# Optimization experiments

Measured on AMD Instinct MI355X. Metric: run time of the kernel, lower is better.

Reference implementation:

```python
import jax, jax.numpy as jnp
import numpy as np

N_ORDERS = 2
CHUNK = 64            # real tokens per chunk
LINEAR_ACTIVATION = False
STAB = 10000.0


def _ensure_stability(x):
    x = jnp.clip(x, -STAB, STAB)
    return jnp.nan_to_num(x, nan=0.0, posinf=STAB, neginf=-STAB)


def setup_inputs() -> dict:
    key = jax.random.key(0)
    k1, k2, k3, k4 = jax.random.split(key, 4)
    B, H, NC, D = 2, 16, 32, 128
    CT = CHUNK * N_ORDERS  # 128 virtual tokens per chunk
    s = 1.0 / np.sqrt(D)
    q_chunks = jax.random.normal(k1, (B, H, NC, CT, D), jnp.float32) * s
    W = jax.random.normal(k2, (B, H, NC, CT, D), jnp.float32) * s
    U = jax.random.normal(k3, (B, H, NC, CT, D), jnp.float32) * s
    h0 = jax.random.normal(k4, (B, H, D, D), jnp.float32) * s
    return {"q_chunks": q_chunks, "W": W, "U": U, "h0": h0}


def _gelu_norm(h):
    # h_norm/2 * gelu(2*h/h_norm, tanh) applied to chunk-boundary state
    n = jnp.linalg.norm(h, axis=-1, keepdims=True) + 1e-6
    return n / 2.0 * jax.nn.gelu(2.0 * h / n, approximate=True)


def _delta_product_scan(q_chunks, W, U, h0):
    B, H, NC, CT, D = q_chunks.shape
    C = CT // N_ORDERS

    def body(h, chunk):
        q_c, w_c, u_c = chunk  # each [B,H,CT,D]
        # virtual-token layout: token c, step s lives at index c*n_orders+s
        qs = q_c.reshape(B, H, C, N_ORDERS, D)
        ws = w_c.reshape(B, H, C, N_ORDERS, D)
        us = u_c.reshape(B, H, C, N_ORDERS, D)
        state = jnp.broadcast_to(h[:, :, None], (B, H, C, D, D))  # per-token state
        outs = []
        for step in range(N_ORDERS):
            q_s = qs[:, :, :, step]
            w_s = ws[:, :, :, step]
            u_s = us[:, :, :, step]
            k_trans_h = jnp.einsum('bhcd,bhcde->bhce', w_s, state)
            u_val = u_s - k_trans_h
            o_inter = jnp.einsum('bhcd,bhcde->bhce', q_s, state)
            o_intra = q_s * u_val  # elementwise, as in source
            outs.append(o_intra + o_inter)
            state = _ensure_stability(state + w_s[..., :, None] * u_val[..., None, :])
        out = jnp.stack(outs, axis=3).reshape(B, H, CT, D)
        h_new = state[:, :, -1]
        if not LINEAR_ACTIVATION:
            h_new = _gelu_norm(h_new)
        return h_new, out

    chunks = (jnp.moveaxis(q_chunks, 2, 0), jnp.moveaxis(W, 2, 0), jnp.moveaxis(U, 2, 0))
    h_final, ys = jax.lax.scan(body, h0, chunks)
    return jnp.moveaxis(ys, 0, 2), h_final  # [B,H,NC,CT,D], [B,H,D,D]


def reference(q_chunks, W, U, h0):
    return _delta_product_scan(q_chunks, W, U, h0)
```

## Files before the change

### kernel.cpp

```cpp
#include <hip/hip_runtime.h>


#define Dd 128
#define NCH 32
#define YS 16777216

typedef __attribute__((ext_vector_type(4))) float floatx4;
typedef __attribute__((ext_vector_type(8))) short short8;

__device__ __forceinline__ unsigned cvtpk(float lo, float hi) {
  unsigned r;
  asm("v_cvt_pk_bf16_f32 %0, %1, %2" : "=v"(r) : "v"(lo), "v"(hi));
  return r;
}

__global__ __launch_bounds__(512) void p1_scan(const float* __restrict__ W,
    const float* __restrict__ U, const float* __restrict__ h0,
    unsigned short* __restrict__ hws, float* __restrict__ out) {
  __shared__ float wpre[NCH * 320];
  __shared__ float upre[NCH * 2 * Dd];
  __shared__ float d10pre[NCH];
  __shared__ float sqb[Dd * 129];
  __shared__ float nrm2[4 * 40];

  const int bh = blockIdx.x;
  const int t = threadIdx.x;
  const int w = t >> 6, l = t & 63;
  const int c = (w << 4) | (l & 15);
  const int rg = l >> 4;

  {
    const float* Wg = W + (size_t)bh * NCH * 16384;
    const float* Ug = U + (size_t)bh * NCH * 16384;
#pragma unroll
    for (int k = 0; k < 4; k++) {
      int idx4 = k * 512 + t;
      int n = idx4 >> 6;
      int rem = idx4 & 63;
      int r = rem >> 5, e4 = (rem & 31) * 4;
      size_t g = (size_t)n * 16384 + (size_t)(126 + r) * Dd + e4;
      *(float4*)&upre[idx4 * 4] = *(const float4*)&Ug[g];
      *(float4*)&wpre[n * 320 + r * 160 + (e4 >> 5) * 40 + (e4 & 31)] =
          *(const float4*)&Wg[g];
    }
  }
  {
    const float4* hg = (const float4*)(h0 + (size_t)bh * 16384);
#pragma unroll
    for (int k = 0; k < 8; k++) {
      int idx4 = k * 512 + t;
      float4 v = hg[idx4];
      int d = idx4 >> 5, e4 = (idx4 & 31) * 4;
      sqb[d * 129 + e4 + 0] = v.x;
      sqb[d * 129 + e4 + 1] = v.y;
      sqb[d * 129 + e4 + 2] = v.z;
      sqb[d * 129 + e4 + 3] = v.w;
    }
  }
  __syncthreads();
  {
    int n = t >> 4, j = t & 15;
    const float* w0p = &wpre[n * 320 + (j >> 2) * 40 + (j & 3) * 8];
    const float* w1p = w0p + 160;
    float p = 0.f;
#pragma unroll
    for (int i = 0; i < 8; i++) p += w0p[i] * w1p[i];
    p += __shfl_xor(p, 1, 64);
    p += __shfl_xor(p, 2, 64);
    p += __shfl_xor(p, 4, 64);
    p += __shfl_xor(p, 8, 64);
    if (j == 0) d10pre[n] = p;
  }
  float hr[32];
#pragma unroll
  for (int i = 0; i < 32; i++) hr[i] = sqb[(rg * 32 + i) * 129 + c];
  __syncthreads();

  const int cpos = (c & 96) | ((c + 8 * rg) & 31);
  float* sqw = &sqb[rg * 32 * 129 + cpos];
  const int srow = t >> 2, sst = t & 3;
  const float* sqr = &sqb[srow * 129 + sst * 32];

  unsigned short* hwsb = hws + (size_t)bh * NCH * 16384;
  {
    unsigned pk[16];
#pragma unroll
    for (int i = 0; i < 16; i++) pk[i] = cvtpk(hr[2 * i], hr[2 * i + 1]);
    uint4* dst = (uint4*)(hwsb + (size_t)c * Dd + rg * 32);
    dst[0] = make_uint4(pk[0], pk[1], pk[2], pk[3]);
    dst[1] = make_uint4(pk[4], pk[5], pk[6], pk[7]);
    dst[2] = make_uint4(pk[8], pk[9], pk[10], pk[11]);
    dst[3] = make_uint4(pk[12], pk[13], pk[14], pk[15]);
  }

  for (int n = 0; n < NCH; n++) {
    floatx4 w0v[8], w1v[8];
    const float* wb = &wpre[n * 320 + rg * 40];
#pragma unroll
    for (int i = 0; i < 8; i++) {
      w0v[i] = *(const floatx4*)&wb[4 * i];
      w1v[i] = *(const floatx4*)&wb[160 + 4 * i];
    }
    float a0 = 0.f, a1 = 0.f, b0 = 0.f, b1 = 0.f;
#pragma unroll
    for (int i = 0; i < 8; i += 2) {
#pragma unroll
      for (int j = 0; j < 4; j++) {
        float h0v = hr[4 * i + j];
        float h1v = hr[4 * i + 4 + j];
        a0 = fmaf(w0v[i][j], h0v, a0);
        a1 = fmaf(w1v[i][j], h0v, a1);
        b0 = fmaf(w0v[i + 1][j], h1v, b0);
        b1 = fmaf(w1v[i + 1][j], h1v, b1);
      }
    }
    a0 += b0; a1 += b1;
    a0 += __shfl_xor(a0, 16, 64);
    a0 += __shfl_xor(a0, 32, 64);
    a1 += __shfl_xor(a1, 16, 64);
    a1 += __shfl_xor(a1, 32, 64);
    const float u0 = upre[n * 256 + c];
    const float u1 = upre[n * 256 + Dd + c];
    const float d10 = d10pre[n];
    const float uv0 = u0 - a0;
    const float uv1 = u1 - a1 - d10 * uv0;
#pragma unroll
    for (int i = 0; i < 8; i++)
#pragma unroll
      for (int j = 0; j < 4; j++) {
        int ii = 4 * i + j;
        float s = __builtin_amdgcn_fmed3f(fmaf(w0v[i][j], uv0, hr[ii]),
                                          -10000.0f, 10000.0f);
        s = __builtin_amdgcn_fmed3f(fmaf(w1v[i][j], uv1, s),
                                    -10000.0f, 10000.0f);
        hr[ii] = s;
        sqw[ii * 129] = s;
      }
    __syncthreads();
    {
      float acc = 0.f, acc2 = 0.f;
#pragma unroll
      for (int b = 0; b < 4; b++) {
        const float* p = sqr + 8 * ((b + sst) & 3);
#pragma unroll
        for (int i = 0; i < 8; i += 2) {
          float v = p[i], v2 = p[i + 1];
          acc = fmaf(v, v, acc);
          acc2 = fmaf(v2, v2, acc2);
        }
      }
      acc += acc2;
      acc += __shfl_xor(acc, 1, 64);
      acc += __shfl_xor(acc, 2, 64);
      if (sst == 0) {
        float nd = sqrtf(acc) + 1e-6f;
        nrm2[(srow >> 5) * 40 + (srow & 31)] = __fdividef(2.0f, nd);
      }
    }
    __syncthreads();
    floatx4 r2v[8];
    const float* nb = &nrm2[rg * 40];
#pragma unroll
    for (int i = 0; i < 8; i++) r2v[i] = *(const floatx4*)&nb[4 * i];
#pragma unroll
    for (int i = 0; i < 8; i++)
#pragma unroll
      for (int j = 0; j < 4; j++) {
        int ii = 4 * i + j;
        float h = hr[ii];
        float x = h * r2v[i][j];
        float x2 = x * x;
        float aa = x * fmaf(0.071354816f, x2, 1.59576912f);
        float ex = __expf(-aa);
        hr[ii] = __fdividef(h, 1.0f + ex);
      }
    if (n < NCH - 1) {
      unsigned pk[16];
#pragma unroll
      for (int i = 0; i < 16; i++) pk[i] = cvtpk(hr[2 * i], hr[2 * i + 1]);
      uint4* dst = (uint4*)(hwsb + (size_t)(n + 1) * 16384 + (size_t)c * Dd + rg * 32);
      dst[0] = make_uint4(pk[0], pk[1], pk[2], pk[3]);
      dst[1] = make_uint4(pk[4], pk[5], pk[6], pk[7]);
      dst[2] = make_uint4(pk[8], pk[9], pk[10], pk[11]);
      dst[3] = make_uint4(pk[12], pk[13], pk[14], pk[15]);
    } else {
      float* ob = out + YS + (size_t)bh * 16384;
#pragma unroll
      for (int i = 0; i < 32; i++) ob[(rg * 32 + i) * Dd + c] = hr[i];
    }
  }
}

__global__ __launch_bounds__(512) void p2_out(const float* __restrict__ Q,
    const float* __restrict__ W, const float* __restrict__ U,
    const unsigned short* __restrict__ hws, float* __restrict__ out) {
  __shared__ unsigned short hT[Dd * 136];
  __shared__ float d10s[64], dq1s[64];
  __shared__ float dps[512];

  const int bid = blockIdx.x;
  const int n = bid & 31, bh = bid >> 5;
  const size_t base = (size_t)(bh * NCH + n) * 16384;
  const float* Qb = Q + base;
  const float* Wb = W + base;
  const float* Ub = U + base;
  float* Ob = out + base;
  const int t = threadIdx.x;

  {
    const uint4* src = (const uint4*)(hws + base);
#pragma unroll
    for (int i = 0; i < 4; i++) {
      int idx = t + i * 512;
      uint4 v = src[idx];
      int e = idx >> 4, j = idx & 15;
      *(uint4*)&hT[e * 136 + j * 8] = v;
    }
  }
  {
    int which = t >> 8, tt = t & 255;
    int cc = tt >> 2, part = tt & 3;
    const float4* ar = (const float4*)((which ? Qb : Wb) + (2 * cc + 1) * Dd + part * 32);
    const float4* w0r = (const float4*)(Wb + (2 * cc) * Dd + part * 32);
    float s = 0.f;
#pragma unroll
    for (int i = 0; i < 8; i++) {
      float4 a = ar[i], b = w0r[i];
      s += a.x * b.x + a.y * b.y + a.z * b.z + a.w * b.w;
    }
    dps[which * 256 + tt] = s;
  }
  __syncthreads();
  if (t < 128) {
    int which = t >> 6, cc = t & 63;
    const float* p = dps + which * 256 + cc * 4;
    float s = p[0] + p[1] + p[2] + p[3];
    (which ? dq1s : d10s)[cc] = s;
  }

  const int wv = t >> 6, l = t & 63;
  const int pr = wv >> 2, eq = wv & 3;
  const int lm = l & 15, lq = l >> 4;

  floatx4 acc[2][4][2];
#pragma unroll
  for (int m = 0; m < 2; m++)
#pragma unroll
    for (int ci = 0; ci < 4; ci++)
#pragma unroll
      for (int j = 0; j < 2; j++) acc[m][ci][j] = (floatx4){0.f, 0.f, 0.f, 0.f};

  for (int kc = 0; kc < 4; kc++) {
    const int k0 = kc * 32;
    short8 bfr[2];
#pragma unroll
    for (int j = 0; j < 2; j++) {
      int ee = (2 * eq + j) * 16 + lm;
      bfr[j] = *(const short8*)&hT[ee * 136 + k0 + 8 * lq];
    }
#pragma unroll
    for (int m = 0; m < 2; m++) {
      const float* X = m ? Wb : Qb;
#pragma unroll
      for (int ci = 0; ci < 4; ci++) {
        int cc = ci * 16 + lm;
        const float* row = X + (size_t)(2 * cc + pr) * Dd + k0 + 8 * lq;
        float4 f0 = ((const float4*)row)[0];
        float4 f1 = ((const float4*)row)[1];
        union { short8 v; unsigned u[4]; } af;
        af.u[0] = cvtpk(f0.x, f0.y);
        af.u[1] = cvtpk(f0.z, f0.w);
        af.u[2] = cvtpk(f1.x, f1.y);
        af.u[3] = cvtpk(f1.z, f1.w);
        acc[m][ci][0] = __builtin_amdgcn_mfma_f32_16x16x32_bf16(af.v, bfr[0], acc[m][ci][0], 0, 0, 0);
        acc[m][ci][1] = __builtin_amdgcn_mfma_f32_16x16x32_bf16(af.v, bfr[1], acc[m][ci][1], 0, 0, 0);
      }
    }
  }
  __syncthreads();
  float* uv0s = (float*)hT;

  if (pr == 0) {
#pragma unroll
    for (int ci = 0; ci < 4; ci++)
#pragma unroll
      for (int j = 0; j < 2; j++) {
        int ee = (2 * eq + j) * 16 + lm;
#pragma unroll
        for (int r = 0; r < 4; r++) {
          int cc = ci * 16 + lq * 4 + r;
          float T0 = acc[1][ci][j][r];
          float Q0h = acc[0][ci][j][r];
          float u0 = Ub[(2 * cc) * Dd + ee];
          float q0 = Qb[(2 * cc) * Dd + ee];
          float uv0 = u0 - T0;
          uv0s[cc * Dd + ee] = uv0;
          Ob[(2 * cc) * Dd + ee] = q0 * uv0 + Q0h;
        }
      }
  }
  __syncthreads();
  if (pr == 1) {
#pragma unroll
    for (int ci = 0; ci < 4; ci++)
#pragma unroll
      for (int j = 0; j < 2; j++) {
        int ee = (2 * eq + j) * 16 + lm;
#pragma unroll
        for (int r = 0; r < 4; r++) {
          int cc = ci * 16 + lq * 4 + r;
          float T1 = acc[1][ci][j][r];
          float Q1h = acc[0][ci][j][r];
          float u1 = Ub[(2 * cc + 1) * Dd + ee];
          float q1 = Qb[(2 * cc + 1) * Dd + ee];
          float uv0 = uv0s[cc * Dd + ee];
          float uv1 = u1 - T1 - d10s[cc] * uv0;
          Ob[(2 * cc + 1) * Dd + ee] = q1 * uv1 + Q1h + dq1s[cc] * uv0;
        }
      }
  }
}

extern "C" void kernel_launch(void* const* d_in, const int* in_sizes, int n_in,
                              void* d_out, int out_size, void* d_ws, size_t ws_size,
                              hipStream_t stream) {
  const float* Q = (const float*)d_in[0];
  const float* W = (const float*)d_in[1];
  const float* U = (const float*)d_in[2];
  const float* h0 = (const float*)d_in[3];
  float* out = (float*)d_out;
  unsigned short* hws = (unsigned short*)d_ws;

  p1_scan<<<32, 512, 0, stream>>>(W, U, h0, hws, out);
  p2_out<<<1024, 512, 0, stream>>>(Q, W, U, hws, out);
}
```

Baseline: 425.7 us.

## Double-buffer Q/W slices into LDS via async global_load_lds in p2_out

The p2_out matmul loop now stages Q and W k-slices into swizzled LDS buffers with async global-to-LDS loads, double-buffered so the next slice loads while the current one feeds MFMA. The odd-row waves now recompute the even-row uv0 with an extra MFMA accumulator instead of exchanging it through shared memory, which removes a block barrier. The aim is to hide global load latency and cut the sync. In exchange it uses more LDS, forces one block per CU through launch bounds, raises register use, and adds redundant MFMA work.

New measurement: 383.3 us. -9.9%, faster.

```diff
diff --git a/kernel.cpp b/kernel.cpp
--- a/kernel.cpp
+++ b/kernel.cpp
@@ -191,10 +191,31 @@
   }
 }
 
-__global__ __launch_bounds__(512) void p2_out(const float* __restrict__ Q,
+
+__device__ __forceinline__ void stage_slice(const float* Qb, const float* Wb,
+    float* qd, float* wd, int kc, int wv6, int ln) {
+#pragma unroll
+  for (int i = 0; i < 4; i++) {
+    int cb = i * 512 + wv6 * 64;
+    int isW = cb >> 10;
+    int cbm = cb & 1023;
+    int c = cbm + ln;
+    int r = c >> 3;
+    int s = (c >> 4) & 7;
+    const float* g = (isW ? Wb : Qb) + r * Dd + kc * 32 + (((c & 7) ^ s) << 2);
+    float* l = (isW ? wd : qd) + (cbm << 2);
+    __builtin_amdgcn_global_load_lds(
+        (const __attribute__((address_space(1))) void*)g,
+        (__attribute__((address_space(3))) void*)l, 16, 0, 0);
+  }
+}
+
+__global__ __launch_bounds__(512, 1) void p2_out(const float* __restrict__ Q,
     const float* __restrict__ W, const float* __restrict__ U,
     const unsigned short* __restrict__ hws, float* __restrict__ out) {
   __shared__ unsigned short hT[Dd * 136];
+  __shared__ float qsl[2][4096];
+  __shared__ float wsl[2][4096];
   __shared__ float d10s[64], dq1s[64];
   __shared__ float dps[512];
 
@@ -206,6 +227,9 @@
   const float* Ub = U + base;
   float* Ob = out + base;
   const int t = threadIdx.x;
+  const int wv6 = t >> 6, ln = t & 63;
+
+  stage_slice(Qb, Wb, &qsl[0][0], &wsl[0][0], 0, wv6, ln);
 
   {
     const uint4* src = (const uint4*)(hws + base);
@@ -238,19 +262,24 @@
     (which ? dq1s : d10s)[cc] = s;
   }
 
-  const int wv = t >> 6, l = t & 63;
-  const int pr = wv >> 2, eq = wv & 3;
-  const int lm = l & 15, lq = l >> 4;
-
-  floatx4 acc[2][4][2];
-#pragma unroll
-  for (int m = 0; m < 2; m++)
+  const int pr = wv6 >> 2, eq = wv6 & 3;
+  const int lm = ln & 15, lq = ln >> 4;
+  const int sw = lm & 7;
+  const int i0 = ((2 * lq) ^ sw) << 2;
+  const int i1 = ((2 * lq + 1) ^ sw) << 2;
+
+  floatx4 acc[3][4][2];
+#pragma unroll
+  for (int m = 0; m < 3; m++)
 #pragma unroll
     for (int ci = 0; ci < 4; ci++)
 #pragma unroll
       for (int j = 0; j < 2; j++) acc[m][ci][j] = (floatx4){0.f, 0.f, 0.f, 0.f};
 
+  int cur = 0;
   for (int kc = 0; kc < 4; kc++) {
+    if (kc < 3)
+      stage_slice(Qb, Wb, &qsl[cur ^ 1][0], &wsl[cur ^ 1][0], kc + 1, wv6, ln);
     const int k0 = kc * 32;
     short8 bfr[2];
 #pragma unroll
@@ -258,27 +287,51 @@
       int ee = (2 * eq + j) * 16 + lm;
       bfr[j] = *(const short8*)&hT[ee * 136 + k0 + 8 * lq];
     }
-#pragma unroll
-    for (int m = 0; m < 2; m++) {
-      const float* X = m ? Wb : Qb;
-#pragma unroll
-      for (int ci = 0; ci < 4; ci++) {
-        int cc = ci * 16 + lm;
-        const float* row = X + (size_t)(2 * cc + pr) * Dd + k0 + 8 * lq;
-        float4 f0 = ((const float4*)row)[0];
-        float4 f1 = ((const float4*)row)[1];
+    const float* qs = &qsl[cur][0];
+    const float* ws = &wsl[cur][0];
+#pragma unroll
+    for (int ci = 0; ci < 4; ci++) {
+      const int rb = (32 * ci + 2 * lm) * 32;
+      {
+        const float* p = qs + rb + pr * 32;
+        floatx4 g0 = *(const floatx4*)(p + i0);
+        floatx4 g1 = *(const floatx4*)(p + i1);
         union { short8 v; unsigned u[4]; } af;
-        af.u[0] = cvtpk(f0.x, f0.y);
-        af.u[1] = cvtpk(f0.z, f0.w);
-        af.u[2] = cvtpk(f1.x, f1.y);
-        af.u[3] = cvtpk(f1.z, f1.w);
-        acc[m][ci][0] = __builtin_amdgcn_mfma_f32_16x16x32_bf16(af.v, bfr[0], acc[m][ci][0], 0, 0, 0);
-        acc[m][ci][1] = __builtin_amdgcn_mfma_f32_16x16x32_bf16(af.v, bfr[1], acc[m][ci][1], 0, 0, 0);
-      }
-    }
-  }
-  __syncthreads();
-  float* uv0s = (float*)hT;
+        af.u[0] = cvtpk(g0[0], g0[1]);
+        af.u[1] = cvtpk(g0[2], g0[3]);
+        af.u[2] = cvtpk(g1[0], g1[1]);
+        af.u[3] = cvtpk(g1[2], g1[3]);
+        acc[0][ci][0] = __builtin_amdgcn_mfma_f32_16x16x32_bf16(af.v, bfr[0], acc[0][ci][0], 0, 0, 0);
+        acc[0][ci][1] = __builtin_amdgcn_mfma_f32_16x16x32_bf16(af.v, bfr[1], acc[0][ci][1], 0, 0, 0);
+      }
+      {
+        const float* p = ws + rb + pr * 32;
+        floatx4 g0 = *(const floatx4*)(p + i0);
+        floatx4 g1 = *(const floatx4*)(p + i1);
+        union { short8 v; unsigned u[4]; } af;
+        af.u[0] = cvtpk(g0[0], g0[1]);
+        af.u[1] = cvtpk(g0[2], g0[3]);
+        af.u[2] = cvtpk(g1[0], g1[1]);
+        af.u[3] = cvtpk(g1[2], g1[3]);
+        acc[1][ci][0] = __builtin_amdgcn_mfma_f32_16x16x32_bf16(af.v, bfr[0], acc[1][ci][0], 0, 0, 0);
+        acc[1][ci][1] = __builtin_amdgcn_mfma_f32_16x16x32_bf16(af.v, bfr[1], acc[1][ci][1], 0, 0, 0);
+      }
+      if (pr) {
+        const float* p = ws + rb;
+        floatx4 g0 = *(const floatx4*)(p + i0);
+        floatx4 g1 = *(const floatx4*)(p + i1);
+        union { short8 v; unsigned u[4]; } af;
+        af.u[0] = cvtpk(g0[0], g0[1]);
+        af.u[1] = cvtpk(g0[2], g0[3]);
+        af.u[2] = cvtpk(g1[0], g1[1]);
+        af.u[3] = cvtpk(g1[2], g1[3]);
+        acc[2][ci][0] = __builtin_amdgcn_mfma_f32_16x16x32_bf16(af.v, bfr[0], acc[2][ci][0], 0, 0, 0);
+        acc[2][ci][1] = __builtin_amdgcn_mfma_f32_16x16x32_bf16(af.v, bfr[1], acc[2][ci][1], 0, 0, 0);
+      }
+    }
+    __syncthreads();
+    cur ^= 1;
+  }
 
   if (pr == 0) {
 #pragma unroll
@@ -294,13 +347,10 @@
           float u0 = Ub[(2 * cc) * Dd + ee];
           float q0 = Qb[(2 * cc) * Dd + ee];
           float uv0 = u0 - T0;
-          uv0s[cc * Dd + ee] = uv0;
           Ob[(2 * cc) * Dd + ee] = q0 * uv0 + Q0h;
         }
       }
-  }
-  __syncthreads();
-  if (pr == 1) {
+  } else {
 #pragma unroll
     for (int ci = 0; ci < 4; ci++)
 #pragma unroll
@@ -311,9 +361,11 @@
           int cc = ci * 16 + lq * 4 + r;
           float T1 = acc[1][ci][j][r];
           float Q1h = acc[0][ci][j][r];
+          float T0 = acc[2][ci][j][r];
+          float u0 = Ub[(2 * cc) * Dd + ee];
           float u1 = Ub[(2 * cc + 1) * Dd + ee];
           float q1 = Qb[(2 * cc + 1) * Dd + ee];
-          float uv0 = uv0s[cc * Dd + ee];
+          float uv0 = u0 - T0;
           float uv1 = u1 - T1 - d10s[cc] * uv0;
           Ob[(2 * cc + 1) * Dd + ee] = q1 * uv1 + Q1h + dq1s[cc] * uv0;
         }
```
